# Kernel tuning notes

Hardware: AMD Instinct MI355X
Metric: run time of the kernel (lower is better)

## Reference

```python
import jax, jax.numpy as jnp
import numpy as np

NEG_SLOPE = 0.2


def gat_layer(x_src, x_dst, src, dst, W, a_src, a_dst, b, n_dst, H, C):
    # Linear transform: [Ns, H, C] / [Nd, H, C]
    h_s = (x_src @ W).reshape(-1, H, C)
    h_d = (x_dst @ W).reshape(-1, H, C)
    # Per-edge attention logits: a . [x_i || x_j] (x_i = dst/target, x_j = src)
    e = jnp.einsum('ehc,hc->eh', h_s[src], a_src) + jnp.einsum('ehc,hc->eh', h_d[dst], a_dst)
    e = jax.nn.leaky_relu(e, NEG_SLOPE)  # [E, H]
    # Segment softmax over destination neighborhoods
    m = jax.ops.segment_max(e, dst, num_segments=n_dst)          # [Nd, H]
    ex = jnp.exp(e - m[dst])
    denom = jax.ops.segment_sum(ex, dst, num_segments=n_dst)    # [Nd, H]
    alpha = ex / denom[dst]                                      # [E, H]
    # Weighted scatter-sum aggregation
    out = jax.ops.segment_sum(alpha[:, :, None] * h_s[src], dst, num_segments=n_dst)
    return out.reshape(n_dst, H * C) + b


def setup_inputs() -> dict:
    key = jax.random.key(0)
    ks = jax.random.split(key, 16)
    N, F_IN, OUT = 200000, 602, 41
    N1, N1D, E1 = 120000, 30000, 960000
    N2D, E2 = 6000, 192000
    s = 0.05
    return {
        'x': jax.random.normal(ks[0], (N, F_IN), jnp.float32),
        'n_id1': jax.random.randint(ks[1], (N1,), 0, N),
        'res_n_id1': jax.random.randint(ks[2], (N1D,), 0, N1),
        'edge_src1': jax.random.randint(ks[3], (E1,), 0, N1),
        'edge_dst1': jax.random.randint(ks[4], (E1,), 0, N1D),
        'res_n_id2': jax.random.randint(ks[5], (N2D,), 0, N1D),
        'edge_src2': jax.random.randint(ks[6], (E2,), 0, N1D),
        'edge_dst2': jax.random.randint(ks[7], (E2,), 0, N2D),
        'W1': jax.random.normal(ks[8], (F_IN, 64), jnp.float32) * s,
        'att_src1': jax.random.normal(ks[9], (8, 8), jnp.float32) * s,
        'att_dst1': jax.random.normal(ks[10], (8, 8), jnp.float32) * s,
        'bias1': jax.random.normal(ks[11], (64,), jnp.float32) * s,
        'W2': jax.random.normal(ks[12], (64, OUT), jnp.float32) * s,
        'att_src2': jax.random.normal(ks[13], (1, OUT), jnp.float32) * s,
        'att_dst2': jax.random.normal(ks[14], (1, OUT), jnp.float32) * s,
        'bias2': jax.random.normal(ks[15], (OUT,), jnp.float32) * s,
    }


def reference(x, n_id1, res_n_id1, edge_src1, edge_dst1, res_n_id2, edge_src2,
              edge_dst2, W1, att_src1, att_dst1, bias1, W2, att_src2, att_dst2, bias2):
    # Block 1: gather frontier, GATConv(in -> 8, heads=8, concat) -> [N1D, 64]
    h = x[n_id1]
    h = gat_layer(h, h[res_n_id1], edge_src1, edge_dst1,
                  W1, att_src1, att_dst1, bias1, res_n_id1.shape[0], 8, 8)
    h = jax.nn.elu(h)
    # (dropout p=0.6 is identity in eval mode)
    # Block 2: GATConv(64 -> out, heads=1) -> [N2D, out]
    h = gat_layer(h, h[res_n_id2], edge_src2, edge_dst2,
                  W2, att_src2, att_dst2, bias2, res_n_id2.shape[0], 1, W2.shape[1])
    return jax.nn.log_softmax(h, axis=1)
```

## Files before the change

### kernel.cpp

```cpp
#include <hip/hip_runtime.h>
#include <hip/hip_bf16.h>
#include <math.h>

typedef __attribute__((ext_vector_type(8))) short short8;
typedef __attribute__((ext_vector_type(4))) float float4v;

__device__ __forceinline__ float wave_max64(float v) {
#pragma unroll
  for (int o = 32; o > 0; o >>= 1) v = fmaxf(v, __shfl_xor(v, o));
  return v;
}
__device__ __forceinline__ float wave_sum64(float v) {
#pragma unroll
  for (int o = 32; o > 0; o >>= 1) v += __shfl_xor(v, o);
  return v;
}
__device__ __forceinline__ float lrelu02(float v) { return v > 0.f ? v : 0.2f * v; }
__device__ __forceinline__ short bf16_rne(float f) {
  unsigned u = __builtin_bit_cast(unsigned, f);
  unsigned r = (u + 0x7FFFu + ((u >> 16) & 1u)) >> 16;
  return (short)r;
}

__global__ void hist_kernel(const int* __restrict__ dst1, const int* __restrict__ dst2,
                            int* __restrict__ counts, int E1, int E2, int N1D) {
  int e = blockIdx.x * blockDim.x + threadIdx.x;
  if (e < E1) atomicAdd(&counts[dst1[e]], 1);
  else if (e < E1 + E2) atomicAdd(&counts[N1D + dst2[e - E1]], 1);
}

__global__ __launch_bounds__(256) void scan1_kernel(const int* __restrict__ counts,
                                                    int* __restrict__ offs,
                                                    int* __restrict__ bsum, int n) {
  __shared__ int ws[4], wpre[4];
  int tid = threadIdx.x, lane = tid & 63, w = tid >> 6;
  int i = blockIdx.x * 256 + tid;
  int v = (i < n) ? counts[i] : 0;
  int x = v;
#pragma unroll
  for (int o = 1; o < 64; o <<= 1) {
    int y = __shfl_up(x, o);
    if (lane >= o) x += y;
  }
  if (lane == 63) ws[w] = x;
  __syncthreads();
  if (tid == 0) {
    int run = 0;
#pragma unroll
    for (int k = 0; k < 4; k++) { wpre[k] = run; run += ws[k]; }
    bsum[blockIdx.x] = run;
  }
  __syncthreads();
  if (i < n) offs[i] = x - v + wpre[w];
}

__global__ __launch_bounds__(256) void scan2_kernel(int* __restrict__ bsum, int nb) {
  __shared__ int ws[4], wpre[4];
  int tid = threadIdx.x, lane = tid & 63, w = tid >> 6;
  int v = (tid < nb) ? bsum[tid] : 0;
  int x = v;
#pragma unroll
  for (int o = 1; o < 64; o <<= 1) {
    int y = __shfl_up(x, o);
    if (lane >= o) x += y;
  }
  if (lane == 63) ws[w] = x;
  __syncthreads();
  if (tid == 0) {
    int run = 0;
#pragma unroll
    for (int k = 0; k < 4; k++) { wpre[k] = run; run += ws[k]; }
  }
  __syncthreads();
  if (tid < nb) bsum[tid] = x - v + wpre[w];
}

__global__ __launch_bounds__(256) void scan3_kernel(int* __restrict__ offs,
                                                    const int* __restrict__ bsum,
                                                    int n, int etot) {
  int i = blockIdx.x * 256 + threadIdx.x;
  if (i < n) offs[i] += bsum[blockIdx.x];
  if (i == 0) offs[n] = etot;
}

__global__ void scatter_kernel(const int* __restrict__ dst1, const int* __restrict__ dst2,
                               const int* __restrict__ offs, int* __restrict__ cursor,
                               int* __restrict__ eidx, int E1, int E2, int N1D) {
  int e = blockIdx.x * blockDim.x + threadIdx.x;
  if (e < E1) {
    int d = dst1[e];
    int pos = offs[d] + atomicAdd(&cursor[d], 1);
    eidx[pos] = e;
  } else if (e < E1 + E2) {
    int e2 = e - E1;
    int d = N1D + dst2[e2];
    int pos = offs[d] + atomicAdd(&cursor[d], 1);
    eidx[pos] = e2;
  }
}

__global__ void prepack_W1_kernel(const float* __restrict__ W, short* __restrict__ Wp) {
  int idx = blockIdx.x * 256 + threadIdx.x;
  if (idx >= 19 * 4 * 64) return;
  int lane = idx & 63;
  int t = (idx >> 6) & 3;
  int s = idx >> 8;
  int quad = lane >> 4, n = t * 16 + (lane & 15);
  short8 v;
#pragma unroll
  for (int j = 0; j < 8; j++) {
    int k = s * 32 + quad * 8 + j;
    v[j] = (k < 602) ? bf16_rne(W[k * 64 + n]) : (short)0;
  }
  *((short8*)Wp + idx) = v;
}

__global__ __launch_bounds__(256) void gemm1_mfma_kernel(const float* __restrict__ x,
                                                         const int* __restrict__ n_id,
                                                         const short* __restrict__ Wp,
                                                         float* __restrict__ out, int M) {
  constexpr int K = 602, NSTEP = 19;
  int tid = threadIdx.x;
  int wid = tid >> 6, lane = tid & 63;
  int quad = lane >> 4, mrow = lane & 15;
  int r = blockIdx.x * 64 + wid * 16 + mrow;
  int grow = n_id[r < M ? r : M - 1];
  const float* xrow = x + (size_t)grow * K;
  float4v acc[4] = {{0.f, 0.f, 0.f, 0.f}, {0.f, 0.f, 0.f, 0.f},
                    {0.f, 0.f, 0.f, 0.f}, {0.f, 0.f, 0.f, 0.f}};
  for (int s = 0; s < NSTEP; s++) {
    int k0 = s * 32 + quad * 8;
    float af[8];
    if (k0 + 8 <= K) {
#pragma unroll
      for (int j = 0; j < 8; j += 2) {
        float2 v = *(const float2*)(xrow + k0 + j);
        af[j] = v.x;
        af[j + 1] = v.y;
      }
    } else {
#pragma unroll
      for (int j = 0; j < 8; j++) af[j] = (k0 + j < K) ? xrow[k0 + j] : 0.f;
    }
    short8 a;
#pragma unroll
    for (int j = 0; j < 8; j++) a[j] = bf16_rne(af[j]);
    const short8* wp = (const short8*)Wp + (size_t)s * 256 + lane;
#pragma unroll
    for (int t = 0; t < 4; t++) {
      short8 b = wp[t * 64];
      acc[t] = __builtin_amdgcn_mfma_f32_16x16x32_bf16(a, b, acc[t], 0, 0, 0);
    }
  }
  int rb = blockIdx.x * 64 + wid * 16;
#pragma unroll
  for (int t = 0; t < 4; t++) {
#pragma unroll
    for (int j = 0; j < 4; j++) {
      int rr = rb + quad * 4 + j;
      if (rr < M) out[(size_t)rr * 64 + t * 16 + mrow] = acc[t][j];
    }
  }
}

__global__ void attn_src1_kernel(const float* __restrict__ hs1, const float* __restrict__ a,
                                 float* __restrict__ s, int N) {
  int t = blockIdx.x * blockDim.x + threadIdx.x;
  if (t >= N * 8) return;
  int i = t >> 3, h = t & 7;
  const float* p = hs1 + (size_t)i * 64 + h * 8;
  const float* q = a + h * 8;
  float acc = 0.f;
#pragma unroll
  for (int j = 0; j < 8; j++) acc += p[j] * q[j];
  s[t] = acc;
}

__global__ void attn_dst1_kernel(const float* __restrict__ hs1, const int* __restrict__ res,
                                 const float* __restrict__ a, float* __restrict__ s, int N) {
  int t = blockIdx.x * blockDim.x + threadIdx.x;
  if (t >= N * 8) return;
  int j = t >> 3, h = t & 7;
  int node = res[j];
  const float* p = hs1 + (size_t)node * 64 + h * 8;
  const float* q = a + h * 8;
  float acc = 0.f;
#pragma unroll
  for (int k = 0; k < 8; k++) acc += p[k] * q[k];
  s[t] = acc;
}

__global__ __launch_bounds__(256) void agg1_kernel(
    const int* __restrict__ offs, const int* __restrict__ eidx, const int* __restrict__ esrc,
    const float* __restrict__ s_src, const float* __restrict__ s_dst,
    const float* __restrict__ hs1, const float* __restrict__ bias,
    float* __restrict__ h1, int n_dst) {
  int wid = (blockIdx.x * blockDim.x + threadIdx.x) >> 6;
  if (wid >= n_dst) return;
  int lane = threadIdx.x & 63;
  int h = lane >> 3;
  float sd = s_dst[wid * 8 + h];
  int beg = offs[wid], end = offs[wid + 1];
  float mx = -1e30f, den = 0.f, acc = 0.f;
  for (int i = beg; i < end; i += 4) {
    int m = end - i; if (m > 4) m = 4;
    int e0[4], sr[4]; float ss[4], row[4];
#pragma unroll
    for (int j = 0; j < 4; j++) e0[j] = eidx[i + (j < m ? j : 0)];
#pragma unroll
    for (int j = 0; j < 4; j++) sr[j] = esrc[e0[j]];
#pragma unroll
    for (int j = 0; j < 4; j++) ss[j] = s_src[sr[j] * 8 + h];
#pragma unroll
    for (int j = 0; j < 4; j++) row[j] = hs1[(size_t)sr[j] * 64 + lane];
    float p[4];
#pragma unroll
    for (int j = 0; j < 4; j++) p[j] = (j < m) ? lrelu02(ss[j] + sd) : -1e30f;
    float bm = mx;
#pragma unroll
    for (int j = 0; j < 4; j++) bm = fmaxf(bm, p[j]);
    float scale = __expf(mx - bm);
    den *= scale;
    acc *= scale;
#pragma unroll
    for (int j = 0; j < 4; j++) {
      float w = __expf(p[j] - bm);
      den += w;
      acc += w * row[j];
    }
    mx = bm;
  }
  float val = (end > beg) ? acc / den : 0.f;
  val += bias[lane];
  val = val > 0.f ? val : __expf(val) - 1.f;
  h1[(size_t)wid * 64 + lane] = val;
}

__global__ __launch_bounds__(256) void gemm2_kernel(const float* __restrict__ h1,
                                                    const float* __restrict__ W2,
                                                    const float* __restrict__ a_src,
                                                    float* __restrict__ hs2,
                                                    float* __restrict__ ssrc, int M) {
  constexpr int C = 41;
  __shared__ float Ws[64 * C];
  for (int i = threadIdx.x; i < 64 * C; i += 256) Ws[i] = W2[i];
  __syncthreads();
  int lane = threadIdx.x & 63;
  int r = blockIdx.x * 4 + (threadIdx.x >> 6);
  if (r >= M) return;
  const float* row = h1 + (size_t)r * 64;
  float acc = 0.f;
  if (lane < C) {
#pragma unroll 8
    for (int k = 0; k < 64; k++) acc += row[k] * Ws[k * C + lane];
  }
  float t = (lane < C) ? acc * a_src[lane] : 0.f;
  t = wave_sum64(t);
  if (lane == 0) ssrc[r] = t;
  if (lane < C) hs2[(size_t)r * C + lane] = acc;
}

__global__ void attn_dst2_kernel(const float* __restrict__ hs2, const int* __restrict__ res,
                                 const float* __restrict__ a, float* __restrict__ s, int N) {
  constexpr int C = 41;
  int wid = (blockIdx.x * blockDim.x + threadIdx.x) >> 6;
  int lane = threadIdx.x & 63;
  if (wid >= N) return;
  int node = res[wid];
  float v = (lane < C) ? hs2[(size_t)node * C + lane] * a[lane] : 0.f;
  v = wave_sum64(v);
  if (lane == 0) s[wid] = v;
}

__global__ __launch_bounds__(256) void agg2_kernel(
    const int* __restrict__ offs, const int* __restrict__ eidx, const int* __restrict__ esrc,
    const float* __restrict__ s_src, const float* __restrict__ s_dst,
    const float* __restrict__ hs2, const float* __restrict__ bias,
    float* __restrict__ out, int n_dst) {
  constexpr int C = 41;
  int wid = (blockIdx.x * blockDim.x + threadIdx.x) >> 6;
  if (wid >= n_dst) return;
  int lane = threadIdx.x & 63;
  bool act = lane < C;
  float sd = s_dst[wid];
  int beg = offs[wid], end = offs[wid + 1];
  float mx = -1e30f, den = 0.f, acc = 0.f;
  for (int i = beg; i < end; i += 4) {
    int m = end - i; if (m > 4) m = 4;
    int e0[4], sr[4]; float ss[4], row[4];
#pragma unroll
    for (int j = 0; j < 4; j++) e0[j] = eidx[i + (j < m ? j : 0)];
#pragma unroll
    for (int j = 0; j < 4; j++) sr[j] = esrc[e0[j]];
#pragma unroll
    for (int j = 0; j < 4; j++) ss[j] = s_src[sr[j]];
#pragma unroll
    for (int j = 0; j < 4; j++) row[j] = act ? hs2[(size_t)sr[j] * C + lane] : 0.f;
    float p[4];
#pragma unroll
    for (int j = 0; j < 4; j++) p[j] = (j < m) ? lrelu02(ss[j] + sd) : -1e30f;
    float bm = mx;
#pragma unroll
    for (int j = 0; j < 4; j++) bm = fmaxf(bm, p[j]);
    float scale = __expf(mx - bm);
    den *= scale;
    acc *= scale;
#pragma unroll
    for (int j = 0; j < 4; j++) {
      float w = __expf(p[j] - bm);
      den += w;
      acc += w * row[j];
    }
    mx = bm;
  }
  float val = (end > beg) ? acc / den : 0.f;
  if (act) val += bias[lane];
  float lv = act ? val : -1e30f;
  float m2 = wave_max64(lv);
  float ex = act ? __expf(val - m2) : 0.f;
  float ssum = wave_sum64(ex);
  if (act) out[(size_t)wid * C + lane] = val - m2 - __logf(ssum);
}

extern "C" void kernel_launch(void* const* d_in, const int* in_sizes, int n_in,
                              void* d_out, int out_size, void* d_ws, size_t ws_size,
                              hipStream_t stream) {
  const float* x    = (const float*)d_in[0];
  const int* n_id1  = (const int*)d_in[1];
  const int* res1   = (const int*)d_in[2];
  const int* esrc1  = (const int*)d_in[3];
  const int* edst1  = (const int*)d_in[4];
  const int* res2   = (const int*)d_in[5];
  const int* esrc2  = (const int*)d_in[6];
  const int* edst2  = (const int*)d_in[7];
  const float* W1   = (const float*)d_in[8];
  const float* as1  = (const float*)d_in[9];
  const float* ad1  = (const float*)d_in[10];
  const float* b1   = (const float*)d_in[11];
  const float* W2   = (const float*)d_in[12];
  const float* as2  = (const float*)d_in[13];
  const float* ad2  = (const float*)d_in[14];
  const float* b2   = (const float*)d_in[15];
  float* out = (float*)d_out;

  const int N1  = in_sizes[1];
  const int N1D = in_sizes[2];
  const int E1  = in_sizes[3];
  const int N2D = in_sizes[5];
  const int E2  = in_sizes[6];
  const int NTOT = N1D + N2D;
  const int ETOT = E1 + E2;

  char* w = (char*)d_ws;
  size_t off = 0;
  auto alloc = [&](size_t bytes) -> void* {
    void* p = (void*)(w + off);
    off += (bytes + 255) & ~(size_t)255;
    return p;
  };
  float* hs1   = (float*)alloc((size_t)N1 * 64 * 4);
  float* ssrc1 = (float*)alloc((size_t)N1 * 8 * 4);
  float* sdst1 = (float*)alloc((size_t)N1D * 8 * 4);
  float* h1    = (float*)alloc((size_t)N1D * 64 * 4);
  float* hs2   = (float*)alloc((size_t)N1D * 41 * 4);
  float* ssrc2 = (float*)alloc((size_t)N1D * 4);
  float* sdst2 = (float*)alloc((size_t)N2D * 4);
  int* counts  = (int*)alloc((size_t)2 * NTOT * 4);
  int* cursor  = counts + NTOT;
  int* offs    = (int*)alloc((size_t)(NTOT + 1) * 4);
  int* bsum    = (int*)alloc((size_t)256 * 4);
  int* eidx    = (int*)alloc((size_t)ETOT * 4);
  short* Wp    = (short*)alloc((size_t)19 * 4 * 64 * 8 * 2);
  (void)ws_size; (void)n_in; (void)out_size;

  hipMemsetAsync(counts, 0, (size_t)2 * NTOT * 4, stream);

  prepack_W1_kernel<<<19, 256, 0, stream>>>(W1, Wp);

  const int nb = (NTOT + 255) / 256;
  hist_kernel<<<(ETOT + 255) / 256, 256, 0, stream>>>(edst1, edst2, counts, E1, E2, N1D);
  scan1_kernel<<<nb, 256, 0, stream>>>(counts, offs, bsum, NTOT);
  scan2_kernel<<<1, 256, 0, stream>>>(bsum, nb);
  scan3_kernel<<<nb, 256, 0, stream>>>(offs, bsum, NTOT, ETOT);
  scatter_kernel<<<(ETOT + 255) / 256, 256, 0, stream>>>(edst1, edst2, offs, cursor, eidx, E1, E2, N1D);

  gemm1_mfma_kernel<<<(N1 + 63) / 64, 256, 0, stream>>>(x, n_id1, Wp, hs1, N1);
  attn_src1_kernel<<<(N1 * 8 + 255) / 256, 256, 0, stream>>>(hs1, as1, ssrc1, N1);
  attn_dst1_kernel<<<(N1D * 8 + 255) / 256, 256, 0, stream>>>(hs1, res1, ad1, sdst1, N1D);
  agg1_kernel<<<(N1D + 3) / 4, 256, 0, stream>>>(offs, eidx, esrc1, ssrc1, sdst1, hs1, b1, h1, N1D);

  gemm2_kernel<<<(N1D + 3) / 4, 256, 0, stream>>>(h1, W2, as2, hs2, ssrc2, N1D);
  attn_dst2_kernel<<<(N2D + 3) / 4, 256, 0, stream>>>(hs2, res2, ad2, sdst2, N2D);
  agg2_kernel<<<(N2D + 3) / 4, 256, 0, stream>>>(offs + N1D, eidx, esrc2, ssrc2, sdst2, hs2, b2, out, N2D);
}
```

Baseline: 872.0 us.

## Fuse small kernels and store source ids directly in CSR payload

```diff
diff --git a/kernel.cpp b/kernel.cpp
--- a/kernel.cpp
+++ b/kernel.cpp
@@ -22,11 +22,29 @@
   return (short)r;
 }
 
-__global__ void hist_kernel(const int* __restrict__ dst1, const int* __restrict__ dst2,
-                            int* __restrict__ counts, int E1, int E2, int N1D) {
-  int e = blockIdx.x * blockDim.x + threadIdx.x;
-  if (e < E1) atomicAdd(&counts[dst1[e]], 1);
-  else if (e < E1 + E2) atomicAdd(&counts[N1D + dst2[e - E1]], 1);
+__global__ void hist_prepack_kernel(const int* __restrict__ dst1, const int* __restrict__ dst2,
+                                    int* __restrict__ counts, const float* __restrict__ W,
+                                    short* __restrict__ Wp, int E1, int E2, int N1D, int nbE) {
+  int b = blockIdx.x;
+  if (b < nbE) {
+    int e = b * 256 + threadIdx.x;
+    if (e < E1) atomicAdd(&counts[dst1[e]], 1);
+    else if (e < E1 + E2) atomicAdd(&counts[N1D + dst2[e - E1]], 1);
+  } else {
+    int idx = (b - nbE) * 256 + threadIdx.x;
+    if (idx >= 19 * 4 * 64) return;
+    int lane = idx & 63;
+    int t = (idx >> 6) & 3;
+    int s = idx >> 8;
+    int quad = lane >> 4, n = t * 16 + (lane & 15);
+    short8 v;
+#pragma unroll
+    for (int j = 0; j < 8; j++) {
+      int k = s * 32 + quad * 8 + j;
+      v[j] = (k < 602) ? bf16_rne(W[k * 64 + n]) : (short)0;
+    }
+    *((short8*)Wp + idx) = v;
+  }
 }
 
 __global__ __launch_bounds__(256) void scan1_kernel(const int* __restrict__ counts,
@@ -83,36 +101,21 @@
   if (i == 0) offs[n] = etot;
 }
 
-__global__ void scatter_kernel(const int* __restrict__ dst1, const int* __restrict__ dst2,
+__global__ void scatter_kernel(const int* __restrict__ dst1, const int* __restrict__ src1,
+                               const int* __restrict__ dst2, const int* __restrict__ src2,
                                const int* __restrict__ offs, int* __restrict__ cursor,
-                               int* __restrict__ eidx, int E1, int E2, int N1D) {
+                               int* __restrict__ epay, int E1, int E2, int N1D) {
   int e = blockIdx.x * blockDim.x + threadIdx.x;
   if (e < E1) {
     int d = dst1[e];
     int pos = offs[d] + atomicAdd(&cursor[d], 1);
-    eidx[pos] = e;
+    epay[pos] = src1[e];
   } else if (e < E1 + E2) {
     int e2 = e - E1;
     int d = N1D + dst2[e2];
     int pos = offs[d] + atomicAdd(&cursor[d], 1);
-    eidx[pos] = e2;
-  }
-}
-
-__global__ void prepack_W1_kernel(const float* __restrict__ W, short* __restrict__ Wp) {
-  int idx = blockIdx.x * 256 + threadIdx.x;
-  if (idx >= 19 * 4 * 64) return;
-  int lane = idx & 63;
-  int t = (idx >> 6) & 3;
-  int s = idx >> 8;
-  int quad = lane >> 4, n = t * 16 + (lane & 15);
-  short8 v;
-#pragma unroll
-  for (int j = 0; j < 8; j++) {
-    int k = s * 32 + quad * 8 + j;
-    v[j] = (k < 602) ? bf16_rne(W[k * 64 + n]) : (short)0;
-  }
-  *((short8*)Wp + idx) = v;
+    epay[pos] = src2[e2];
+  }
 }
 
 __global__ __launch_bounds__(256) void gemm1_mfma_kernel(const float* __restrict__ x,
@@ -176,54 +179,43 @@
   s[t] = acc;
 }
 
-__global__ void attn_dst1_kernel(const float* __restrict__ hs1, const int* __restrict__ res,
-                                 const float* __restrict__ a, float* __restrict__ s, int N) {
-  int t = blockIdx.x * blockDim.x + threadIdx.x;
-  if (t >= N * 8) return;
-  int j = t >> 3, h = t & 7;
-  int node = res[j];
-  const float* p = hs1 + (size_t)node * 64 + h * 8;
-  const float* q = a + h * 8;
-  float acc = 0.f;
-#pragma unroll
-  for (int k = 0; k < 8; k++) acc += p[k] * q[k];
-  s[t] = acc;
-}
-
 __global__ __launch_bounds__(256) void agg1_kernel(
-    const int* __restrict__ offs, const int* __restrict__ eidx, const int* __restrict__ esrc,
-    const float* __restrict__ s_src, const float* __restrict__ s_dst,
-    const float* __restrict__ hs1, const float* __restrict__ bias,
-    float* __restrict__ h1, int n_dst) {
+    const int* __restrict__ offs, const int* __restrict__ srcs,
+    const float* __restrict__ s_src, const int* __restrict__ res,
+    const float* __restrict__ ad, const float* __restrict__ hs1,
+    const float* __restrict__ bias, float* __restrict__ h1, int n_dst) {
   int wid = (blockIdx.x * blockDim.x + threadIdx.x) >> 6;
   if (wid >= n_dst) return;
   int lane = threadIdx.x & 63;
   int h = lane >> 3;
-  float sd = s_dst[wid * 8 + h];
+  int node = res[wid];
+  float v = hs1[(size_t)node * 64 + lane] * ad[lane];
+  v += __shfl_xor(v, 1);
+  v += __shfl_xor(v, 2);
+  v += __shfl_xor(v, 4);
+  float sd = v;
   int beg = offs[wid], end = offs[wid + 1];
   float mx = -1e30f, den = 0.f, acc = 0.f;
-  for (int i = beg; i < end; i += 4) {
-    int m = end - i; if (m > 4) m = 4;
-    int e0[4], sr[4]; float ss[4], row[4];
-#pragma unroll
-    for (int j = 0; j < 4; j++) e0[j] = eidx[i + (j < m ? j : 0)];
-#pragma unroll
-    for (int j = 0; j < 4; j++) sr[j] = esrc[e0[j]];
-#pragma unroll
-    for (int j = 0; j < 4; j++) ss[j] = s_src[sr[j] * 8 + h];
-#pragma unroll
-    for (int j = 0; j < 4; j++) row[j] = hs1[(size_t)sr[j] * 64 + lane];
-    float p[4];
-#pragma unroll
-    for (int j = 0; j < 4; j++) p[j] = (j < m) ? lrelu02(ss[j] + sd) : -1e30f;
+  for (int i = beg; i < end; i += 8) {
+    int m = end - i; if (m > 8) m = 8;
+    int sr[8]; float ss[8], row[8];
+#pragma unroll
+    for (int j = 0; j < 8; j++) sr[j] = srcs[i + (j < m ? j : 0)];
+#pragma unroll
+    for (int j = 0; j < 8; j++) ss[j] = s_src[sr[j] * 8 + h];
+#pragma unroll
+    for (int j = 0; j < 8; j++) row[j] = hs1[(size_t)sr[j] * 64 + lane];
+    float p[8];
+#pragma unroll
+    for (int j = 0; j < 8; j++) p[j] = (j < m) ? lrelu02(ss[j] + sd) : -1e30f;
     float bm = mx;
 #pragma unroll
-    for (int j = 0; j < 4; j++) bm = fmaxf(bm, p[j]);
+    for (int j = 0; j < 8; j++) bm = fmaxf(bm, p[j]);
     float scale = __expf(mx - bm);
     den *= scale;
     acc *= scale;
 #pragma unroll
-    for (int j = 0; j < 4; j++) {
+    for (int j = 0; j < 8; j++) {
       float w = __expf(p[j] - bm);
       den += w;
       acc += w * row[j];
@@ -260,53 +252,41 @@
   if (lane < C) hs2[(size_t)r * C + lane] = acc;
 }
 
-__global__ void attn_dst2_kernel(const float* __restrict__ hs2, const int* __restrict__ res,
-                                 const float* __restrict__ a, float* __restrict__ s, int N) {
-  constexpr int C = 41;
-  int wid = (blockIdx.x * blockDim.x + threadIdx.x) >> 6;
-  int lane = threadIdx.x & 63;
-  if (wid >= N) return;
-  int node = res[wid];
-  float v = (lane < C) ? hs2[(size_t)node * C + lane] * a[lane] : 0.f;
-  v = wave_sum64(v);
-  if (lane == 0) s[wid] = v;
-}
-
 __global__ __launch_bounds__(256) void agg2_kernel(
-    const int* __restrict__ offs, const int* __restrict__ eidx, const int* __restrict__ esrc,
-    const float* __restrict__ s_src, const float* __restrict__ s_dst,
-    const float* __restrict__ hs2, const float* __restrict__ bias,
-    float* __restrict__ out, int n_dst) {
+    const int* __restrict__ offs, const int* __restrict__ srcs,
+    const float* __restrict__ s_src, const int* __restrict__ res,
+    const float* __restrict__ ad, const float* __restrict__ hs2,
+    const float* __restrict__ bias, float* __restrict__ out, int n_dst) {
   constexpr int C = 41;
   int wid = (blockIdx.x * blockDim.x + threadIdx.x) >> 6;
   if (wid >= n_dst) return;
   int lane = threadIdx.x & 63;
   bool act = lane < C;
-  float sd = s_dst[wid];
+  int node = res[wid];
+  float dv = act ? hs2[(size_t)node * C + lane] * ad[lane] : 0.f;
+  float sd = wave_sum64(dv);
   int beg = offs[wid], end = offs[wid + 1];
   float mx = -1e30f, den = 0.f, acc = 0.f;
-  for (int i = beg; i < end; i += 4) {
-    int m = end - i; if (m > 4) m = 4;
-    int e0[4], sr[4]; float ss[4], row[4];
-#pragma unroll
-    for (int j = 0; j < 4; j++) e0[j] = eidx[i + (j < m ? j : 0)];
-#pragma unroll
-    for (int j = 0; j < 4; j++) sr[j] = esrc[e0[j]];
-#pragma unroll
-    for (int j = 0; j < 4; j++) ss[j] = s_src[sr[j]];
-#pragma unroll
-    for (int j = 0; j < 4; j++) row[j] = act ? hs2[(size_t)sr[j] * C + lane] : 0.f;
-    float p[4];
-#pragma unroll
-    for (int j = 0; j < 4; j++) p[j] = (j < m) ? lrelu02(ss[j] + sd) : -1e30f;
+  for (int i = beg; i < end; i += 8) {
+    int m = end - i; if (m > 8) m = 8;
+    int sr[8]; float ss[8], row[8];
+#pragma unroll
+    for (int j = 0; j < 8; j++) sr[j] = srcs[i + (j < m ? j : 0)];
+#pragma unroll
+    for (int j = 0; j < 8; j++) ss[j] = s_src[sr[j]];
+#pragma unroll
+    for (int j = 0; j < 8; j++) row[j] = act ? hs2[(size_t)sr[j] * C + lane] : 0.f;
+    float p[8];
+#pragma unroll
+    for (int j = 0; j < 8; j++) p[j] = (j < m) ? lrelu02(ss[j] + sd) : -1e30f;
     float bm = mx;
 #pragma unroll
-    for (int j = 0; j < 4; j++) bm = fmaxf(bm, p[j]);
+    for (int j = 0; j < 8; j++) bm = fmaxf(bm, p[j]);
     float scale = __expf(mx - bm);
     den *= scale;
     acc *= scale;
 #pragma unroll
-    for (int j = 0; j < 4; j++) {
+    for (int j = 0; j < 8; j++) {
       float w = __expf(p[j] - bm);
       den += w;
       acc += w * row[j];
@@ -360,36 +340,31 @@
   };
   float* hs1   = (float*)alloc((size_t)N1 * 64 * 4);
   float* ssrc1 = (float*)alloc((size_t)N1 * 8 * 4);
-  float* sdst1 = (float*)alloc((size_t)N1D * 8 * 4);
   float* h1    = (float*)alloc((size_t)N1D * 64 * 4);
   float* hs2   = (float*)alloc((size_t)N1D * 41 * 4);
   float* ssrc2 = (float*)alloc((size_t)N1D * 4);
-  float* sdst2 = (float*)alloc((size_t)N2D * 4);
   int* counts  = (int*)alloc((size_t)2 * NTOT * 4);
   int* cursor  = counts + NTOT;
   int* offs    = (int*)alloc((size_t)(NTOT + 1) * 4);
   int* bsum    = (int*)alloc((size_t)256 * 4);
-  int* eidx    = (int*)alloc((size_t)ETOT * 4);
+  int* epay    = (int*)alloc((size_t)ETOT * 4);
   short* Wp    = (short*)alloc((size_t)19 * 4 * 64 * 8 * 2);
   (void)ws_size; (void)n_in; (void)out_size;
 
   hipMemsetAsync(counts, 0, (size_t)2 * NTOT * 4, stream);
 
-  prepack_W1_kernel<<<19, 256, 0, stream>>>(W1, Wp);
-
+  const int nbE = (ETOT + 255) / 256;
   const int nb = (NTOT + 255) / 256;
-  hist_kernel<<<(ETOT + 255) / 256, 256, 0, stream>>>(edst1, edst2, counts, E1, E2, N1D);
+  hist_prepack_kernel<<<nbE + 19, 256, 0, stream>>>(edst1, edst2, counts, W1, Wp, E1, E2, N1D, nbE);
   scan1_kernel<<<nb, 256, 0, stream>>>(counts, offs, bsum, NTOT);
   scan2_kernel<<<1, 256, 0, stream>>>(bsum, nb);
   scan3_kernel<<<nb, 256, 0, stream>>>(offs, bsum, NTOT, ETOT);
-  scatter_kernel<<<(ETOT + 255) / 256, 256, 0, stream>>>(edst1, edst2, offs, cursor, eidx, E1, E2, N1D);
+  scatter_kernel<<<nbE, 256, 0, stream>>>(edst1, esrc1, edst2, esrc2, offs, cursor, epay, E1, E2, N1D);
 
   gemm1_mfma_kernel<<<(N1 + 63) / 64, 256, 0, stream>>>(x, n_id1, Wp, hs1, N1);
   attn_src1_kernel<<<(N1 * 8 + 255) / 256, 256, 0, stream>>>(hs1, as1, ssrc1, N1);
-  attn_dst1_kernel<<<(N1D * 8 + 255) / 256, 256, 0, stream>>>(hs1, res1, ad1, sdst1, N1D);
-  agg1_kernel<<<(N1D + 3) / 4, 256, 0, stream>>>(offs, eidx, esrc1, ssrc1, sdst1, hs1, b1, h1, N1D);
+  agg1_kernel<<<(N1D + 3) / 4, 256, 0, stream>>>(offs, epay, ssrc1, res1, ad1, hs1, b1, h1, N1D);
 
   gemm2_kernel<<<(N1D + 3) / 4, 256, 0, stream>>>(h1, W2, as2, hs2, ssrc2, N1D);
-  attn_dst2_kernel<<<(N2D + 3) / 4, 256, 0, stream>>>(hs2, res2, ad2, sdst2, N2D);
-  agg2_kernel<<<(N2D + 3) / 4, 256, 0, stream>>>(offs + N1D, eidx, esrc2, ssrc2, sdst2, hs2, b2, out, N2D);
-}
+  agg2_kernel<<<(N2D + 3) / 4, 256, 0, stream>>>(offs + N1D, epay, ssrc2, res2, ad2, hs2, b2, out, N2D);
+}
```

Result: faster. 840.4 us (-3.6%).
